# Kernel tuning notes

Hardware: AMD Instinct MI355X
Metric: run time of the kernel (lower is better)

The kernel has to match this reference:

```python
import jax, jax.numpy as jnp
import numpy as np

TS = 0.1
ECNUM = 1024
CA1NUM = 1024
CA3NUM = 1024
CA3SIGMA = 5.0
TRACKLEN = 100
ACTNUM = 2
BS = 8192
CUELOC = int(0.1 * TRACKLEN)  # sensory cue injected at this step
NOISE_P = 0.04 * TS           # per-step EC3 spontaneous-spike probability


def _xavier_std(fan_in, fan_out):
    return float(np.sqrt(2.0 / (fan_in + fan_out)))


def setup_inputs() -> dict:
    key = jax.random.key(0)
    ks = jax.random.split(key, 6)
    cue = jax.random.normal(ks[0], (BS, ECNUM), jnp.float32)
    ec5_init = jax.random.uniform(ks[1], (BS, ECNUM), jnp.float32)
    wca3ca1 = jax.random.uniform(ks[2], (CA3NUM, CA1NUM), jnp.float32) * 0.01
    wec3ca1 = jax.random.normal(ks[3], (ECNUM, CA1NUM), jnp.float32) * _xavier_std(ECNUM, CA1NUM)
    wca1ec5 = jax.random.normal(ks[4], (CA1NUM, ECNUM), jnp.float32) * _xavier_std(CA1NUM, ECNUM)
    wca1act = jax.random.normal(ks[5], (CA1NUM, ACTNUM), jnp.float32) * _xavier_std(CA1NUM, ACTNUM)
    ca1bias = jnp.zeros((CA1NUM,), jnp.float32)
    ec5bias = jnp.zeros((ECNUM,), jnp.float32)
    actbias = jnp.zeros((ACTNUM,), jnp.float32)
    return {"cue": cue, "ec5_init": ec5_init, "wca3ca1": wca3ca1,
            "wec3ca1": wec3ca1, "wca1ec5": wca1ec5, "wca1act": wca1act,
            "ca1bias": ca1bias, "ec5bias": ec5bias, "actbias": actbias}


def _forward(cue, ec5_init, wca3ca1, wec3ca1, wca1ec5, wca1act, ca1bias, ec5bias, actbias):
    bs = cue.shape[0]
    dt = cue.dtype
    # CA3 place-cell tuning curves for all positions: (T, ca3num)
    ca3center = jnp.linspace(0.0, TRACKLEN, CA3NUM).astype(dt)
    xs = jnp.arange(TRACKLEN)
    ca3_all = jnp.exp(-((ca3center[None, :] - xs[:, None].astype(dt)) ** 2)
                      / (2.0 * CA3SIGMA ** 2))
    drive = ca3_all @ wca3ca1            # (T, ca1num), precomputed CA3->CA1 drive
    cue_mask = (xs == CUELOC).astype(dt)  # (T,)
    noise_key = jax.random.key(42)

    ec3_0 = jnp.zeros((bs, ECNUM), dt)
    ca1_0 = jnp.zeros((bs, CA1NUM), dt)

    def step(carry, inp):
        ec3, ec5, _ = carry
        d, m, t = inp
        ca1 = jax.nn.relu(d[None, :] * (1.0 + jax.nn.sigmoid(ec3 @ wec3ca1)) - ca1bias)
        ec5 = ec5 + (10.0 * TS) * (ca1 @ wca1ec5) + ec5bias
        ec5 = 0.5 + 0.5 * jax.nn.sigmoid(4.0 * (ec5 - 0.5))
        ec3 = ec5 * ec3 + m * cue
        k = jax.random.fold_in(noise_key, t)
        ec3 = ec3 + 0.2 * jax.random.bernoulli(k, NOISE_P, (bs, ECNUM)).astype(dt)
        return (ec3, ec5, ca1), None

    (ec3, ec5, ca1), _ = jax.lax.scan(step, (ec3_0, ec5_init, ca1_0),
                                      (drive, cue_mask, xs))
    return ca1 @ wca1act + actbias       # (bs, actnum)


def reference(cue, ec5_init, wca3ca1, wec3ca1, wca1ec5, wca1act, ca1bias, ec5bias, actbias):
    return _forward(cue, ec5_init, wca3ca1, wec3ca1, wca1ec5, wca1act,
                    ca1bias, ec5bias, actbias)
```

## Files before the change

### kernel.cpp

```cpp
#include <hip/hip_runtime.h>
#include <stdint.h>

#define BS 8192
#define NDIM 1024
#define T_STEPS 100
#define CUE_T 10
#define BK 64
#define NKT (NDIM / BK)

typedef __attribute__((ext_vector_type(8))) short bf16x8;
typedef __attribute__((ext_vector_type(16))) float f32x16;

__device__ inline uint16_t f32_to_bf16(float f) {
    uint32_t u = __float_as_uint(f);
    uint32_t r = u + 0x7fffu + ((u >> 16) & 1u);
    return (uint16_t)(r >> 16);
}
__device__ inline float bf16_to_f32(uint16_t h) {
    return __uint_as_float(((uint32_t)h) << 16);
}

__host__ __device__ inline uint32_t rotl32_(uint32_t x, uint32_t r) {
    return (x << r) | (x >> (32u - r));
}

__host__ __device__ inline void tf2x32(uint32_t k0, uint32_t k1,
                                       uint32_t x0, uint32_t x1,
                                       uint32_t &o0, uint32_t &o1) {
    uint32_t ks2 = k0 ^ k1 ^ 0x1BD11BDAu;
    x0 += k0; x1 += k1;
#define TF_R4(a,b,c,d) \
    x0 += x1; x1 = rotl32_(x1,(a)); x1 ^= x0; \
    x0 += x1; x1 = rotl32_(x1,(b)); x1 ^= x0; \
    x0 += x1; x1 = rotl32_(x1,(c)); x1 ^= x0; \
    x0 += x1; x1 = rotl32_(x1,(d)); x1 ^= x0;
    TF_R4(13,15,26,6)  x0 += k1;  x1 += ks2 + 1u;
    TF_R4(17,29,16,24) x0 += ks2; x1 += k0 + 2u;
    TF_R4(13,15,26,6)  x0 += k0;  x1 += k1 + 3u;
    TF_R4(17,29,16,24) x0 += k1;  x1 += ks2 + 4u;
    TF_R4(13,15,26,6)  x0 += ks2; x1 += k0 + 5u;
#undef TF_R4
    o0 = x0; o1 = x1;
}

__device__ __forceinline__ void tf2x32_x4_fold(uint32_t k0, uint32_t k1,
                                               const uint32_t idx[4],
                                               uint32_t bits[4]) {
    uint32_t ks2 = k0 ^ k1 ^ 0x1BD11BDAu;
    uint32_t x0[4], x1[4];
    #pragma unroll
    for (int i = 0; i < 4; ++i) { x0[i] = k0; x1[i] = idx[i] + k1; }
#define TF4_R(rot) \
    _Pragma("unroll") \
    for (int i = 0; i < 4; ++i) { \
        x0[i] += x1[i]; x1[i] = rotl32_(x1[i], (rot)); x1[i] ^= x0[i]; }
#define TF4_K(a0, a1) \
    _Pragma("unroll") \
    for (int i = 0; i < 4; ++i) { x0[i] += (a0); x1[i] += (a1); }
    TF4_R(13) TF4_R(15) TF4_R(26) TF4_R(6)  TF4_K(k1, ks2 + 1u)
    TF4_R(17) TF4_R(29) TF4_R(16) TF4_R(24) TF4_K(ks2, k0 + 2u)
    TF4_R(13) TF4_R(15) TF4_R(26) TF4_R(6)  TF4_K(k0, k1 + 3u)
    TF4_R(17) TF4_R(29) TF4_R(16) TF4_R(24) TF4_K(k1, ks2 + 4u)
    TF4_R(13) TF4_R(15) TF4_R(26) TF4_R(6)  TF4_K(ks2, k0 + 5u)
#undef TF4_R
#undef TF4_K
    #pragma unroll
    for (int i = 0; i < 4; ++i) bits[i] = x0[i] ^ x1[i];
}

__device__ inline float sigmoidf_(float x) {
    float e = __expf(-x);
    return __builtin_amdgcn_rcpf(1.0f + e);
}

__device__ __forceinline__ void gload16(const uint16_t* g, uint16_t* l) {
    __builtin_amdgcn_global_load_lds(
        (const __attribute__((address_space(1))) void*)g,
        (__attribute__((address_space(3))) void*)l, 16, 0, 0);
}

__global__ void init_kernel(const float* __restrict__ ec5_init,
                            uint16_t* __restrict__ ec3bf,
                            uint16_t* __restrict__ ec5bf, int n) {
    int i = blockIdx.x * blockDim.x + threadIdx.x;
    if (i < n) { ec3bf[i] = 0; ec5bf[i] = f32_to_bf16(ec5_init[i]); }
}

__global__ __launch_bounds__(256) void drive_kernel(const float* __restrict__ W,
                                                    float* __restrict__ drive) {
    __shared__ float g[4][1024];
    const int t0 = blockIdx.x * 4;
    const int c = blockIdx.y * 64 + (threadIdx.x & 63);
    const int tt = threadIdx.x >> 6;
    const float stepf = 100.0f / 1023.0f;
    for (int i = threadIdx.x; i < 4096; i += 256) {
        int t_ = i >> 10, j = i & 1023;
        float d = stepf * (float)j - (float)(t0 + t_);
        g[t_][j] = expf(-(d * d) * 0.02f);
    }
    __syncthreads();
    float a = 0.f;
    for (int j = 0; j < 1024; ++j)
        a = fmaf(g[tt][j], W[(size_t)j * NDIM + c], a);
    drive[(size_t)(t0 + tt) * NDIM + c] = a;
}

__global__ __launch_bounds__(256) void wtrans_kernel(const float* __restrict__ W,
                                                     uint16_t* __restrict__ Wt) {
    __shared__ float tile[32][33];
    int k0 = blockIdx.x * 32, n0 = blockIdx.y * 32;
    int tx = threadIdx.x & 31, ty = threadIdx.x >> 5;
    #pragma unroll
    for (int i = 0; i < 32; i += 8)
        tile[ty + i][tx] = W[(size_t)(k0 + ty + i) * NDIM + n0 + tx];
    __syncthreads();
    #pragma unroll
    for (int i = 0; i < 32; i += 8)
        Wt[(size_t)(n0 + ty + i) * NDIM + k0 + tx] = f32_to_bf16(tile[tx][ty + i]);
}

template<bool NOISE>
__device__ __forceinline__ void gemm_core_t(const uint16_t* __restrict__ A,
                                            const uint16_t* __restrict__ Bt,
                                            uint16_t* As, uint16_t* Bs,
                                            f32x16 acc[2][2],
                                            uint32_t k0_, uint32_t k1_,
                                            uint32_t obase, uint64_t &mask) {
    const int tid = threadIdx.x;
    const int wid = tid >> 6, lane = tid & 63;
    const int row0 = blockIdx.x * 128, col0 = blockIdx.y * 128;
    const int srow = lane >> 3;
    const int soff = ((lane & 7) ^ srow) * 8;
    const uint16_t* aS[4]; const uint16_t* bS[4];
    #pragma unroll
    for (int i = 0; i < 4; ++i) {
        int ch = wid * 4 + i;
        aS[i] = A  + (size_t)(row0 + ch * 8 + srow) * NDIM + soff;
        bS[i] = Bt + (size_t)(col0 + ch * 8 + srow) * NDIM + soff;
    }
    const int l31 = lane & 31, l5 = lane >> 5;
    const int wr = wid >> 1, wc = wid & 1;
    int aoff[2][4], boff[2][4];
    #pragma unroll
    for (int m = 0; m < 2; ++m)
        #pragma unroll
        for (int kk = 0; kk < 4; ++kk) {
            int ar = wr * 64 + m * 32 + l31;
            aoff[m][kk] = ar * BK + ((((kk << 1) | l5) ^ (ar & 7)) << 3);
            int br = wc * 64 + m * 32 + l31;
            boff[m][kk] = br * BK + ((((kk << 1) | l5) ^ (br & 7)) << 3);
        }

    #pragma unroll
    for (int i = 0; i < 4; ++i) {
        int ch = wid * 4 + i;
        gload16(aS[i], As + ch * 512);
        gload16(bS[i], Bs + ch * 512);
    }

    for (int kt = 0; kt < NKT; ++kt) {
        const int cur = kt & 1;
        if (kt + 1 < NKT) {
            const int nb = (cur ^ 1) * 8192;
            const int k0n = (kt + 1) * BK;
            #pragma unroll
            for (int i = 0; i < 4; ++i) {
                int ch = wid * 4 + i;
                gload16(aS[i] + k0n, As + nb + ch * 512);
                gload16(bS[i] + k0n, Bs + nb + ch * 512);
            }
            asm volatile("s_waitcnt vmcnt(8)" ::: "memory");
        } else {
            asm volatile("s_waitcnt vmcnt(0)" ::: "memory");
        }
        __builtin_amdgcn_s_barrier();
        __builtin_amdgcn_sched_barrier(0);
        const uint16_t* as = As + cur * 8192;
        const uint16_t* bs = Bs + cur * 8192;
        bf16x8 af[2][4], bfr[2][4];
        #pragma unroll
        for (int m = 0; m < 2; ++m)
            #pragma unroll
            for (int kk = 0; kk < 4; ++kk) {
                af[m][kk]  = *(const bf16x8*)&as[aoff[m][kk]];
                bfr[m][kk] = *(const bf16x8*)&bs[boff[m][kk]];
            }
        #pragma unroll
        for (int kk = 0; kk < 4; ++kk)
            #pragma unroll
            for (int m = 0; m < 2; ++m)
                #pragma unroll
                for (int n = 0; n < 2; ++n)
                    acc[m][n] = __builtin_amdgcn_mfma_f32_32x32x16_bf16(
                        af[m][kk], bfr[n][kk], acc[m][n], 0, 0, 0);
        if (NOISE) {
            uint32_t idx[4], bits[4];
            const uint32_t base = obase + (uint32_t)((kt >> 1) << 14)
                                + (uint32_t)((kt & 1) << 2);
            #pragma unroll
            for (int u = 0; u < 4; ++u) idx[u] = base + u;
            tf2x32_x4_fold(k0_, k1_, idx, bits);
            #pragma unroll
            for (int u = 0; u < 4; ++u) {
                float uu = __uint_as_float((bits[u] >> 9) | 0x3f800000u) - 1.0f;
                mask |= (uint64_t)(uu < 0.004f ? 1u : 0u) << ((kt << 2) + u);
            }
        }
        __builtin_amdgcn_sched_barrier(0);
        __builtin_amdgcn_s_barrier();
    }
}

__device__ __forceinline__ void acc_to_lds(float* lacc, f32x16 acc[2][2]) {
    const int tid = threadIdx.x, wid = tid >> 6, lane = tid & 63;
    const int wr = wid >> 1, wc = wid & 1, l31 = lane & 31, l5 = lane >> 5;
    #pragma unroll
    for (int m = 0; m < 2; ++m)
        #pragma unroll
        for (int n = 0; n < 2; ++n) {
            int c = wc * 64 + n * 32 + l31;
            int chunk = c >> 2, cj = c & 3;
            #pragma unroll
            for (int e = 0; e < 16; ++e) {
                int r = wr * 64 + m * 32 + (e & 3) + ((e >> 2) << 3) + (l5 << 2);
                lacc[r * 128 + ((chunk ^ (r & 31)) << 2) + cj] = acc[m][n][e];
            }
        }
}

__device__ __forceinline__ void acc_read8(const float* lacc, int r, int a,
                                          float4 &v0, float4 &v1) {
    int rb = r & 31;
    v0 = *(const float4*)&lacc[r * 128 + ((((a << 1) | 0) ^ rb) << 2)];
    v1 = *(const float4*)&lacc[r * 128 + ((((a << 1) | 1) ^ rb) << 2)];
}

__global__ __launch_bounds__(256, 2) void gemm1_kernel(
    const uint16_t* __restrict__ ec3bf, const uint16_t* __restrict__ W1t,
    const float* __restrict__ drv, const float* __restrict__ bias,
    uint16_t* __restrict__ ca1bf, float* __restrict__ ca1f, int writef32,
    uint64_t* __restrict__ maskbuf, uint32_t k0_, uint32_t k1_)
{
    __shared__ __align__(16) uint16_t SM[2][16384];
    uint16_t* As = SM[0];
    uint16_t* Bs = SM[1];
    f32x16 acc[2][2];
    #pragma unroll
    for (int m = 0; m < 2; ++m)
        #pragma unroll
        for (int n = 0; n < 2; ++n)
            acc[m][n] = (f32x16)(0.0f);

    const int tid = threadIdx.x;
    const int row0 = blockIdx.x * 128, col0 = blockIdx.y * 128;
    const int a = tid & 15;
    const uint32_t obase = (uint32_t)(row0 + (tid >> 4)) * NDIM
                         + (uint32_t)(col0 + a * 8);
    uint64_t mask = 0;
    gemm_core_t<true>(ec3bf, W1t, As, Bs, acc, k0_, k1_, obase, mask);

    maskbuf[(size_t)(blockIdx.y * 64 + blockIdx.x) * 256 + tid] = mask;

    float* lacc = (float*)SM;
    acc_to_lds(lacc, acc);
    __syncthreads();

    #pragma unroll
    for (int i = 0; i < 8; ++i) {
        int r = (tid >> 4) + i * 16;
        float4 v0, v1;
        acc_read8(lacc, r, a, v0, v1);
        int gc = col0 + a * 8;
        float4 d0 = *(const float4*)&drv[gc];
        float4 d1 = *(const float4*)&drv[gc + 4];
        float4 b0 = *(const float4*)&bias[gc];
        float4 b1 = *(const float4*)&bias[gc + 4];
        size_t off = (size_t)(row0 + r) * NDIM + gc;
        float vout[8];
        #pragma unroll
        for (int j = 0; j < 8; ++j) {
            float accv = j < 4 ? v0[j] : v1[j - 4];
            float dv = j < 4 ? d0[j] : d1[j - 4];
            float bi = j < 4 ? b0[j] : b1[j - 4];
            float s = sigmoidf_(accv);
            float v = dv * (1.0f + s) - bi;
            vout[j] = v > 0.0f ? v : 0.0f;
        }
        bf16x8 pk;
        #pragma unroll
        for (int j = 0; j < 8; ++j) pk[j] = (short)f32_to_bf16(vout[j]);
        *(bf16x8*)&ca1bf[off] = pk;
        if (writef32) {
            float4 f0 = {vout[0], vout[1], vout[2], vout[3]};
            float4 f1 = {vout[4], vout[5], vout[6], vout[7]};
            *(float4*)&ca1f[off] = f0;
            *(float4*)&ca1f[off + 4] = f1;
        }
    }
}

__global__ __launch_bounds__(256, 2) void gemm2_kernel(
    const uint16_t* __restrict__ ca1bf, const uint16_t* __restrict__ W2t,
    const float* __restrict__ cue, const float* __restrict__ bias,
    uint16_t* __restrict__ ec3bf, uint16_t* __restrict__ ec5bf,
    const uint64_t* __restrict__ maskbuf, int inject)
{
    __shared__ __align__(16) uint16_t SM[2][16384];
    uint16_t* As = SM[0];
    uint16_t* Bs = SM[1];
    f32x16 acc[2][2];
    #pragma unroll
    for (int m = 0; m < 2; ++m)
        #pragma unroll
        for (int n = 0; n < 2; ++n)
            acc[m][n] = (f32x16)(0.0f);

    const int tid = threadIdx.x;
    const int row0 = blockIdx.x * 128, col0 = blockIdx.y * 128;
    const int a = tid & 15;
    const uint64_t mask = maskbuf[(size_t)(blockIdx.y * 64 + blockIdx.x) * 256 + tid];

    uint64_t dummy = 0;
    gemm_core_t<false>(ca1bf, W2t, As, Bs, acc, 0u, 0u, 0u, dummy);

    bf16x8 e3v[8], e5v[8];
    #pragma unroll
    for (int i = 0; i < 8; ++i) {
        size_t off = (size_t)(row0 + (tid >> 4) + i * 16) * NDIM + col0 + a * 8;
        e3v[i] = *(const bf16x8*)&ec3bf[off];
        e5v[i] = *(const bf16x8*)&ec5bf[off];
    }

    float* lacc = (float*)SM;
    acc_to_lds(lacc, acc);
    __syncthreads();

    #pragma unroll
    for (int i = 0; i < 8; ++i) {
        int r = (tid >> 4) + i * 16;
        float4 v0, v1;
        acc_read8(lacc, r, a, v0, v1);
        int gc = col0 + a * 8;
        size_t off = (size_t)(row0 + r) * NDIM + gc;
        float4 b0 = *(const float4*)&bias[gc];
        float4 b1 = *(const float4*)&bias[gc + 4];
        float4 c0 = {0.f,0.f,0.f,0.f}, c1 = {0.f,0.f,0.f,0.f};
        if (inject) {
            c0 = *(const float4*)&cue[off];
            c1 = *(const float4*)&cue[off + 4];
        }
        bf16x8 p3, p5;
        #pragma unroll
        for (int j = 0; j < 8; ++j) {
            float accv = j < 4 ? v0[j] : v1[j - 4];
            float bi = j < 4 ? b0[j] : b1[j - 4];
            float e5 = bf16_to_f32((uint16_t)e5v[i][j]);
            float e3 = bf16_to_f32((uint16_t)e3v[i][j]);
            float u = e5 + accv + bi;
            float e5n = 0.5f + 0.5f * sigmoidf_(4.0f * (u - 0.5f));
            float e3n = e5n * e3;
            if (inject) e3n += (j < 4 ? c0[j] : c1[j - 4]);
            e3n += ((mask >> (i * 8 + j)) & 1ull) ? 0.2f : 0.0f;
            p5[j] = (short)f32_to_bf16(e5n);
            p3[j] = (short)f32_to_bf16(e3n);
        }
        *(bf16x8*)&ec5bf[off] = p5;
        *(bf16x8*)&ec3bf[off] = p3;
    }
}

__global__ __launch_bounds__(256) void final_kernel(
    const float* __restrict__ ca1,
    const float* __restrict__ wact,
    const float* __restrict__ actbias,
    float* __restrict__ out)
{
    int wave = threadIdx.x >> 6, lane = threadIdx.x & 63;
    int b = blockIdx.x * 4 + wave;
    double a0 = 0.0, a1 = 0.0;
    for (int c = lane; c < NDIM; c += 64) {
        double v = (double)ca1[(size_t)b * NDIM + c];
        a0 += v * (double)wact[c * 2 + 0];
        a1 += v * (double)wact[c * 2 + 1];
    }
    #pragma unroll
    for (int off = 32; off > 0; off >>= 1) {
        a0 += __shfl_down(a0, off);
        a1 += __shfl_down(a1, off);
    }
    if (lane == 0) {
        out[(size_t)b * 2 + 0] = (float)(a0 + (double)actbias[0]);
        out[(size_t)b * 2 + 1] = (float)(a1 + (double)actbias[1]);
    }
}

extern "C" void kernel_launch(void* const* d_in, const int* in_sizes, int n_in,
                              void* d_out, int out_size, void* d_ws, size_t ws_size,
                              hipStream_t stream) {
    const float* cue      = (const float*)d_in[0];
    const float* ec5_init = (const float*)d_in[1];
    const float* wca3ca1  = (const float*)d_in[2];
    const float* wec3ca1  = (const float*)d_in[3];
    const float* wca1ec5  = (const float*)d_in[4];
    const float* wca1act  = (const float*)d_in[5];
    const float* ca1bias  = (const float*)d_in[6];
    const float* ec5bias  = (const float*)d_in[7];
    const float* actbias  = (const float*)d_in[8];
    float* out = (float*)d_out;

    const size_t NE = (size_t)BS * NDIM;
    char* p = (char*)d_ws;
    float*    ca1f    = (float*)p;    p += NE * 4;
    uint16_t* ec3bf   = (uint16_t*)p; p += NE * 2;
    uint16_t* ec5bf   = (uint16_t*)p; p += NE * 2;
    uint16_t* ca1bf   = (uint16_t*)p; p += NE * 2;
    uint16_t* W1t     = (uint16_t*)p; p += (size_t)NDIM * NDIM * 2;
    uint16_t* W2t     = (uint16_t*)p; p += (size_t)NDIM * NDIM * 2;
    uint64_t* maskbuf = (uint64_t*)p; p += (size_t)512 * 256 * 8;
    float*    drive   = (float*)p;

    const int n = (int)NE;
    hipLaunchKernelGGL(init_kernel, dim3((n + 255) / 256), dim3(256), 0, stream,
                       ec5_init, ec3bf, ec5bf, n);
    hipLaunchKernelGGL(drive_kernel, dim3(25, 16), dim3(256), 0, stream,
                       wca3ca1, drive);
    hipLaunchKernelGGL(wtrans_kernel, dim3(32, 32), dim3(256), 0, stream, wec3ca1, W1t);
    hipLaunchKernelGGL(wtrans_kernel, dim3(32, 32), dim3(256), 0, stream, wca1ec5, W2t);

    dim3 blk(256);
    dim3 gg(BS / 128, NDIM / 128);
    for (int t = 0; t < T_STEPS; ++t) {
        uint32_t k0, k1;
        tf2x32(0u, 42u, 0u, (uint32_t)t, k0, k1);
        hipLaunchKernelGGL(gemm1_kernel, gg, blk, 0, stream,
                           ec3bf, W1t, drive + (size_t)t * NDIM, ca1bias,
                           ca1bf, ca1f, (t == T_STEPS - 1) ? 1 : 0,
                           maskbuf, k0, k1);
        if (t < T_STEPS - 1) {
            hipLaunchKernelGGL(gemm2_kernel, gg, blk, 0, stream,
                               ca1bf, W2t, cue, ec5bias, ec3bf, ec5bf,
                               maskbuf, (t == CUE_T) ? 1 : 0);
        }
    }
    hipLaunchKernelGGL(final_kernel, dim3(BS / 4), blk, 0, stream,
                       ca1f, wca1act, actbias, out);
}
```

Measured before the change: 6.308 ms.

## Fuse all timesteps into one persistent cooperative kernel with grid syncs

Replaces the 199 per-step GEMM launches with one cooperative persistent kernel of 512 blocks. Each block loops over all timesteps, running both GEMMs and their epilogues, with grid.sync between phases. The Bernoulli noise mask now stays in registers instead of round-tripping through a global buffer. To fit 4 blocks per CU, the LDS double buffering is removed, so k-tile loads are no longer overlapped with MFMA and the epilogue runs in two half-tile passes. This trades launch overhead for lost load/compute overlap and grid-barrier cost.

```diff
diff --git a/kernel.cpp b/kernel.cpp
--- a/kernel.cpp
+++ b/kernel.cpp
@@ -1,5 +1,8 @@
 #include <hip/hip_runtime.h>
+#include <hip/hip_cooperative_groups.h>
 #include <stdint.h>
+
+namespace cg = cooperative_groups;
 
 #define BS 8192
 #define NDIM 1024
@@ -119,25 +122,50 @@
         Wt[(size_t)(n0 + ty + i) * NDIM + k0 + tx] = f32_to_bf16(tile[tx][ty + i]);
 }
 
-template<bool NOISE>
-__device__ __forceinline__ void gemm_core_t(const uint16_t* __restrict__ A,
-                                            const uint16_t* __restrict__ Bt,
-                                            uint16_t* As, uint16_t* Bs,
-                                            f32x16 acc[2][2],
-                                            uint32_t k0_, uint32_t k1_,
-                                            uint32_t obase, uint64_t &mask) {
+__device__ __forceinline__ void acc_pass_to_lds(float* lacc, f32x16 acc[2][2],
+                                                int p, int wr, int wc,
+                                                int l31, int l5) {
+    #pragma unroll
+    for (int n = 0; n < 2; ++n) {
+        int c = wc * 64 + n * 32 + l31;
+        int chunk = c >> 2, cj = c & 3;
+        #pragma unroll
+        for (int e = 0; e < 16; ++e) {
+            int rlow = (e & 3) + ((e >> 2) << 3) + (l5 << 2);
+            lacc[(wr * 32 + rlow) * 128 + ((chunk ^ rlow) << 2) + cj] = acc[p][n][e];
+        }
+    }
+}
+
+__device__ __forceinline__ void acc_read8(const float* lacc, int rp, int a,
+                                          float4 &v0, float4 &v1) {
+    int rb = rp & 31;
+    v0 = *(const float4*)&lacc[rp * 128 + ((((a << 1) | 0) ^ rb) << 2)];
+    v1 = *(const float4*)&lacc[rp * 128 + ((((a << 1) | 1) ^ rb) << 2)];
+}
+
+__global__ __launch_bounds__(256, 4) void fused_kernel(
+    uint16_t* __restrict__ ec3bf, uint16_t* __restrict__ ec5bf,
+    uint16_t* __restrict__ ca1bf,
+    const uint16_t* __restrict__ W1t, const uint16_t* __restrict__ W2t,
+    const float* __restrict__ drive, const float* __restrict__ ca1bias,
+    const float* __restrict__ ec5bias, const float* __restrict__ cue,
+    float* __restrict__ ca1f)
+{
+    cg::grid_group grid = cg::this_grid();
+    __shared__ __align__(16) uint16_t SM[16384];
+    uint16_t* As = SM;
+    uint16_t* Bs = SM + 8192;
+    float* lacc = (float*)SM;
+
     const int tid = threadIdx.x;
     const int wid = tid >> 6, lane = tid & 63;
-    const int row0 = blockIdx.x * 128, col0 = blockIdx.y * 128;
+    const int blin = blockIdx.x;
+    const int bx = blin & 63, by = blin >> 6;
+    const int row0 = bx * 128, col0 = by * 128;
+
     const int srow = lane >> 3;
     const int soff = ((lane & 7) ^ srow) * 8;
-    const uint16_t* aS[4]; const uint16_t* bS[4];
-    #pragma unroll
-    for (int i = 0; i < 4; ++i) {
-        int ch = wid * 4 + i;
-        aS[i] = A  + (size_t)(row0 + ch * 8 + srow) * NDIM + soff;
-        bS[i] = Bt + (size_t)(col0 + ch * 8 + srow) * NDIM + soff;
-    }
     const int l31 = lane & 31, l5 = lane >> 5;
     const int wr = wid >> 1, wc = wid & 1;
     int aoff[2][4], boff[2][4];
@@ -151,221 +179,212 @@
             boff[m][kk] = br * BK + ((((kk << 1) | l5) ^ (br & 7)) << 3);
         }
 
-    #pragma unroll
-    for (int i = 0; i < 4; ++i) {
-        int ch = wid * 4 + i;
-        gload16(aS[i], As + ch * 512);
-        gload16(bS[i], Bs + ch * 512);
-    }
-
-    for (int kt = 0; kt < NKT; ++kt) {
-        const int cur = kt & 1;
-        if (kt + 1 < NKT) {
-            const int nb = (cur ^ 1) * 8192;
-            const int k0n = (kt + 1) * BK;
+    const int a = tid & 15;
+    const int gc = col0 + a * 8;
+    const uint32_t obase = (uint32_t)(row0 + (tid >> 4)) * NDIM + (uint32_t)gc;
+    const float4 cb0 = *(const float4*)&ca1bias[gc];
+    const float4 cb1 = *(const float4*)&ca1bias[gc + 4];
+    const float4 eb0 = *(const float4*)&ec5bias[gc];
+    const float4 eb1 = *(const float4*)&ec5bias[gc + 4];
+
+    static const int passA[4] = {0, 1, 4, 5};
+    static const int passB[4] = {2, 3, 6, 7};
+
+    for (int t = 0; t < T_STEPS; ++t) {
+        uint32_t k0_, k1_;
+        tf2x32(0u, 42u, 0u, (uint32_t)t, k0_, k1_);
+        const float* drv = drive + (size_t)t * NDIM;
+
+        f32x16 acc[2][2];
+        #pragma unroll
+        for (int m = 0; m < 2; ++m)
+            #pragma unroll
+            for (int n = 0; n < 2; ++n)
+                acc[m][n] = (f32x16)(0.0f);
+        uint64_t mask = 0;
+
+        const uint16_t* aS[4]; const uint16_t* bS[4];
+        #pragma unroll
+        for (int i = 0; i < 4; ++i) {
+            int ch = wid * 4 + i;
+            aS[i] = ec3bf + (size_t)(row0 + ch * 8 + srow) * NDIM + soff;
+            bS[i] = W1t   + (size_t)(col0 + ch * 8 + srow) * NDIM + soff;
+        }
+        for (int kt = 0; kt < NKT; ++kt) {
+            if (kt) __builtin_amdgcn_s_barrier();
+            const int k0n = kt * BK;
             #pragma unroll
             for (int i = 0; i < 4; ++i) {
                 int ch = wid * 4 + i;
-                gload16(aS[i] + k0n, As + nb + ch * 512);
-                gload16(bS[i] + k0n, Bs + nb + ch * 512);
+                gload16(aS[i] + k0n, As + ch * 512);
+                gload16(bS[i] + k0n, Bs + ch * 512);
             }
-            asm volatile("s_waitcnt vmcnt(8)" ::: "memory");
-        } else {
+            {
+                uint32_t idx[4], bits[4];
+                const uint32_t base = obase + (uint32_t)((kt >> 1) << 14)
+                                    + (uint32_t)((kt & 1) << 2);
+                #pragma unroll
+                for (int u = 0; u < 4; ++u) idx[u] = base + u;
+                tf2x32_x4_fold(k0_, k1_, idx, bits);
+                #pragma unroll
+                for (int u = 0; u < 4; ++u) {
+                    float uu = __uint_as_float((bits[u] >> 9) | 0x3f800000u) - 1.0f;
+                    mask |= (uint64_t)(uu < 0.004f ? 1u : 0u) << ((kt << 2) + u);
+                }
+            }
             asm volatile("s_waitcnt vmcnt(0)" ::: "memory");
-        }
-        __builtin_amdgcn_s_barrier();
-        __builtin_amdgcn_sched_barrier(0);
-        const uint16_t* as = As + cur * 8192;
-        const uint16_t* bs = Bs + cur * 8192;
-        bf16x8 af[2][4], bfr[2][4];
+            __builtin_amdgcn_s_barrier();
+            __builtin_amdgcn_sched_barrier(0);
+            bf16x8 af[2][4], bfr[2][4];
+            #pragma unroll
+            for (int m = 0; m < 2; ++m)
+                #pragma unroll
+                for (int kk = 0; kk < 4; ++kk) {
+                    af[m][kk]  = *(const bf16x8*)&As[aoff[m][kk]];
+                    bfr[m][kk] = *(const bf16x8*)&Bs[boff[m][kk]];
+                }
+            #pragma unroll
+            for (int kk = 0; kk < 4; ++kk)
+                #pragma unroll
+                for (int m = 0; m < 2; ++m)
+                    #pragma unroll
+                    for (int n = 0; n < 2; ++n)
+                        acc[m][n] = __builtin_amdgcn_mfma_f32_32x32x16_bf16(
+                            af[m][kk], bfr[n][kk], acc[m][n], 0, 0, 0);
+            __builtin_amdgcn_sched_barrier(0);
+        }
+
+        const float4 d0 = *(const float4*)&drv[gc];
+        const float4 d1 = *(const float4*)&drv[gc + 4];
+        #pragma unroll
+        for (int p = 0; p < 2; ++p) {
+            __syncthreads();
+            acc_pass_to_lds(lacc, acc, p, wr, wc, l31, l5);
+            __syncthreads();
+            const int* il = p ? passB : passA;
+            #pragma unroll
+            for (int ii = 0; ii < 4; ++ii) {
+                int i = il[ii];
+                int r = (tid >> 4) + i * 16;
+                int rp = ((r >> 6) << 5) | (r & 31);
+                float4 v0, v1;
+                acc_read8(lacc, rp, a, v0, v1);
+                size_t off = (size_t)(row0 + r) * NDIM + gc;
+                float vout[8];
+                #pragma unroll
+                for (int j = 0; j < 8; ++j) {
+                    float accv = j < 4 ? v0[j] : v1[j - 4];
+                    float dv = j < 4 ? d0[j] : d1[j - 4];
+                    float bi = j < 4 ? cb0[j] : cb1[j - 4];
+                    float s = sigmoidf_(accv);
+                    float v = dv * (1.0f + s) - bi;
+                    vout[j] = v > 0.0f ? v : 0.0f;
+                }
+                bf16x8 pk;
+                #pragma unroll
+                for (int j = 0; j < 8; ++j) pk[j] = (short)f32_to_bf16(vout[j]);
+                *(bf16x8*)&ca1bf[off] = pk;
+                if (t == T_STEPS - 1) {
+                    float4 f0 = {vout[0], vout[1], vout[2], vout[3]};
+                    float4 f1 = {vout[4], vout[5], vout[6], vout[7]};
+                    *(float4*)&ca1f[off] = f0;
+                    *(float4*)&ca1f[off + 4] = f1;
+                }
+            }
+        }
+        if (t == T_STEPS - 1) break;
+        grid.sync();
+
         #pragma unroll
         for (int m = 0; m < 2; ++m)
             #pragma unroll
-            for (int kk = 0; kk < 4; ++kk) {
-                af[m][kk]  = *(const bf16x8*)&as[aoff[m][kk]];
-                bfr[m][kk] = *(const bf16x8*)&bs[boff[m][kk]];
+            for (int n = 0; n < 2; ++n)
+                acc[m][n] = (f32x16)(0.0f);
+        #pragma unroll
+        for (int i = 0; i < 4; ++i) {
+            int ch = wid * 4 + i;
+            aS[i] = ca1bf + (size_t)(row0 + ch * 8 + srow) * NDIM + soff;
+            bS[i] = W2t   + (size_t)(col0 + ch * 8 + srow) * NDIM + soff;
+        }
+        for (int kt = 0; kt < NKT; ++kt) {
+            if (kt) __builtin_amdgcn_s_barrier();
+            const int k0n = kt * BK;
+            #pragma unroll
+            for (int i = 0; i < 4; ++i) {
+                int ch = wid * 4 + i;
+                gload16(aS[i] + k0n, As + ch * 512);
+                gload16(bS[i] + k0n, Bs + ch * 512);
             }
-        #pragma unroll
-        for (int kk = 0; kk < 4; ++kk)
+            asm volatile("s_waitcnt vmcnt(0)" ::: "memory");
+            __builtin_amdgcn_s_barrier();
+            __builtin_amdgcn_sched_barrier(0);
+            bf16x8 af[2][4], bfr[2][4];
             #pragma unroll
             for (int m = 0; m < 2; ++m)
                 #pragma unroll
-                for (int n = 0; n < 2; ++n)
-                    acc[m][n] = __builtin_amdgcn_mfma_f32_32x32x16_bf16(
-                        af[m][kk], bfr[n][kk], acc[m][n], 0, 0, 0);
-        if (NOISE) {
-            uint32_t idx[4], bits[4];
-            const uint32_t base = obase + (uint32_t)((kt >> 1) << 14)
-                                + (uint32_t)((kt & 1) << 2);
-            #pragma unroll
-            for (int u = 0; u < 4; ++u) idx[u] = base + u;
-            tf2x32_x4_fold(k0_, k1_, idx, bits);
-            #pragma unroll
-            for (int u = 0; u < 4; ++u) {
-                float uu = __uint_as_float((bits[u] >> 9) | 0x3f800000u) - 1.0f;
-                mask |= (uint64_t)(uu < 0.004f ? 1u : 0u) << ((kt << 2) + u);
+                for (int kk = 0; kk < 4; ++kk) {
+                    af[m][kk]  = *(const bf16x8*)&As[aoff[m][kk]];
+                    bfr[m][kk] = *(const bf16x8*)&Bs[boff[m][kk]];
+                }
+            #pragma unroll
+            for (int kk = 0; kk < 4; ++kk)
+                #pragma unroll
+                for (int m = 0; m < 2; ++m)
+                    #pragma unroll
+                    for (int n = 0; n < 2; ++n)
+                        acc[m][n] = __builtin_amdgcn_mfma_f32_32x32x16_bf16(
+                            af[m][kk], bfr[n][kk], acc[m][n], 0, 0, 0);
+            __builtin_amdgcn_sched_barrier(0);
+        }
+
+        bf16x8 e3v[8], e5v[8];
+        #pragma unroll
+        for (int i = 0; i < 8; ++i) {
+            size_t off = (size_t)(row0 + (tid >> 4) + i * 16) * NDIM + gc;
+            e3v[i] = *(const bf16x8*)&ec3bf[off];
+            e5v[i] = *(const bf16x8*)&ec5bf[off];
+        }
+
+        const int inject = (t == CUE_T);
+        #pragma unroll
+        for (int p = 0; p < 2; ++p) {
+            __syncthreads();
+            acc_pass_to_lds(lacc, acc, p, wr, wc, l31, l5);
+            __syncthreads();
+            const int* il = p ? passB : passA;
+            #pragma unroll
+            for (int ii = 0; ii < 4; ++ii) {
+                int i = il[ii];
+                int r = (tid >> 4) + i * 16;
+                int rp = ((r >> 6) << 5) | (r & 31);
+                float4 v0, v1;
+                acc_read8(lacc, rp, a, v0, v1);
+                size_t off = (size_t)(row0 + r) * NDIM + gc;
+                float4 c0 = {0.f,0.f,0.f,0.f}, c1 = {0.f,0.f,0.f,0.f};
+                if (inject) {
+                    c0 = *(const float4*)&cue[off];
+                    c1 = *(const float4*)&cue[off + 4];
+                }
+                bf16x8 p3, p5;
+                #pragma unroll
+                for (int j = 0; j < 8; ++j) {
+                    float accv = j < 4 ? v0[j] : v1[j - 4];
+                    float bi = j < 4 ? eb0[j] : eb1[j - 4];
+                    float e5 = bf16_to_f32((uint16_t)e5v[i][j]);
+                    float e3 = bf16_to_f32((uint16_t)e3v[i][j]);
+                    float u = e5 + accv + bi;
+                    float e5n = 0.5f + 0.5f * sigmoidf_(4.0f * (u - 0.5f));
+                    float e3n = e5n * e3;
+                    if (inject) e3n += (j < 4 ? c0[j] : c1[j - 4]);
+                    e3n += ((mask >> (i * 8 + j)) & 1ull) ? 0.2f : 0.0f;
+                    p5[j] = (short)f32_to_bf16(e5n);
+                    p3[j] = (short)f32_to_bf16(e3n);
+                }
+                *(bf16x8*)&ec5bf[off] = p5;
+                *(bf16x8*)&ec3bf[off] = p3;
             }
         }
-        __builtin_amdgcn_sched_barrier(0);
-        __builtin_amdgcn_s_barrier();
-    }
-}
-
-__device__ __forceinline__ void acc_to_lds(float* lacc, f32x16 acc[2][2]) {
-    const int tid = threadIdx.x, wid = tid >> 6, lane = tid & 63;
-    const int wr = wid >> 1, wc = wid & 1, l31 = lane & 31, l5 = lane >> 5;
-    #pragma unroll
-    for (int m = 0; m < 2; ++m)
-        #pragma unroll
-        for (int n = 0; n < 2; ++n) {
-            int c = wc * 64 + n * 32 + l31;
-            int chunk = c >> 2, cj = c & 3;
-            #pragma unroll
-            for (int e = 0; e < 16; ++e) {
-                int r = wr * 64 + m * 32 + (e & 3) + ((e >> 2) << 3) + (l5 << 2);
-                lacc[r * 128 + ((chunk ^ (r & 31)) << 2) + cj] = acc[m][n][e];
-            }
-        }
-}
-
-__device__ __forceinline__ void acc_read8(const float* lacc, int r, int a,
-                                          float4 &v0, float4 &v1) {
-    int rb = r & 31;
-    v0 = *(const float4*)&lacc[r * 128 + ((((a << 1) | 0) ^ rb) << 2)];
-    v1 = *(const float4*)&lacc[r * 128 + ((((a << 1) | 1) ^ rb) << 2)];
-}
-
-__global__ __launch_bounds__(256, 2) void gemm1_kernel(
-    const uint16_t* __restrict__ ec3bf, const uint16_t* __restrict__ W1t,
-    const float* __restrict__ drv, const float* __restrict__ bias,
-    uint16_t* __restrict__ ca1bf, float* __restrict__ ca1f, int writef32,
-    uint64_t* __restrict__ maskbuf, uint32_t k0_, uint32_t k1_)
-{
-    __shared__ __align__(16) uint16_t SM[2][16384];
-    uint16_t* As = SM[0];
-    uint16_t* Bs = SM[1];
-    f32x16 acc[2][2];
-    #pragma unroll
-    for (int m = 0; m < 2; ++m)
-        #pragma unroll
-        for (int n = 0; n < 2; ++n)
-            acc[m][n] = (f32x16)(0.0f);
-
-    const int tid = threadIdx.x;
-    const int row0 = blockIdx.x * 128, col0 = blockIdx.y * 128;
-    const int a = tid & 15;
-    const uint32_t obase = (uint32_t)(row0 + (tid >> 4)) * NDIM
-                         + (uint32_t)(col0 + a * 8);
-    uint64_t mask = 0;
-    gemm_core_t<true>(ec3bf, W1t, As, Bs, acc, k0_, k1_, obase, mask);
-
-    maskbuf[(size_t)(blockIdx.y * 64 + blockIdx.x) * 256 + tid] = mask;
-
-    float* lacc = (float*)SM;
-    acc_to_lds(lacc, acc);
-    __syncthreads();
-
-    #pragma unroll
-    for (int i = 0; i < 8; ++i) {
-        int r = (tid >> 4) + i * 16;
-        float4 v0, v1;
-        acc_read8(lacc, r, a, v0, v1);
-        int gc = col0 + a * 8;
-        float4 d0 = *(const float4*)&drv[gc];
-        float4 d1 = *(const float4*)&drv[gc + 4];
-        float4 b0 = *(const float4*)&bias[gc];
-        float4 b1 = *(const float4*)&bias[gc + 4];
-        size_t off = (size_t)(row0 + r) * NDIM + gc;
-        float vout[8];
-        #pragma unroll
-        for (int j = 0; j < 8; ++j) {
-            float accv = j < 4 ? v0[j] : v1[j - 4];
-            float dv = j < 4 ? d0[j] : d1[j - 4];
-            float bi = j < 4 ? b0[j] : b1[j - 4];
-            float s = sigmoidf_(accv);
-            float v = dv * (1.0f + s) - bi;
-            vout[j] = v > 0.0f ? v : 0.0f;
-        }
-        bf16x8 pk;
-        #pragma unroll
-        for (int j = 0; j < 8; ++j) pk[j] = (short)f32_to_bf16(vout[j]);
-        *(bf16x8*)&ca1bf[off] = pk;
-        if (writef32) {
-            float4 f0 = {vout[0], vout[1], vout[2], vout[3]};
-            float4 f1 = {vout[4], vout[5], vout[6], vout[7]};
-            *(float4*)&ca1f[off] = f0;
-            *(float4*)&ca1f[off + 4] = f1;
-        }
-    }
-}
-
-__global__ __launch_bounds__(256, 2) void gemm2_kernel(
-    const uint16_t* __restrict__ ca1bf, const uint16_t* __restrict__ W2t,
-    const float* __restrict__ cue, const float* __restrict__ bias,
-    uint16_t* __restrict__ ec3bf, uint16_t* __restrict__ ec5bf,
-    const uint64_t* __restrict__ maskbuf, int inject)
-{
-    __shared__ __align__(16) uint16_t SM[2][16384];
-    uint16_t* As = SM[0];
-    uint16_t* Bs = SM[1];
-    f32x16 acc[2][2];
-    #pragma unroll
-    for (int m = 0; m < 2; ++m)
-        #pragma unroll
-        for (int n = 0; n < 2; ++n)
-            acc[m][n] = (f32x16)(0.0f);
-
-    const int tid = threadIdx.x;
-    const int row0 = blockIdx.x * 128, col0 = blockIdx.y * 128;
-    const int a = tid & 15;
-    const uint64_t mask = maskbuf[(size_t)(blockIdx.y * 64 + blockIdx.x) * 256 + tid];
-
-    uint64_t dummy = 0;
-    gemm_core_t<false>(ca1bf, W2t, As, Bs, acc, 0u, 0u, 0u, dummy);
-
-    bf16x8 e3v[8], e5v[8];
-    #pragma unroll
-    for (int i = 0; i < 8; ++i) {
-        size_t off = (size_t)(row0 + (tid >> 4) + i * 16) * NDIM + col0 + a * 8;
-        e3v[i] = *(const bf16x8*)&ec3bf[off];
-        e5v[i] = *(const bf16x8*)&ec5bf[off];
-    }
-
-    float* lacc = (float*)SM;
-    acc_to_lds(lacc, acc);
-    __syncthreads();
-
-    #pragma unroll
-    for (int i = 0; i < 8; ++i) {
-        int r = (tid >> 4) + i * 16;
-        float4 v0, v1;
-        acc_read8(lacc, r, a, v0, v1);
-        int gc = col0 + a * 8;
-        size_t off = (size_t)(row0 + r) * NDIM + gc;
-        float4 b0 = *(const float4*)&bias[gc];
-        float4 b1 = *(const float4*)&bias[gc + 4];
-        float4 c0 = {0.f,0.f,0.f,0.f}, c1 = {0.f,0.f,0.f,0.f};
-        if (inject) {
-            c0 = *(const float4*)&cue[off];
-            c1 = *(const float4*)&cue[off + 4];
-        }
-        bf16x8 p3, p5;
-        #pragma unroll
-        for (int j = 0; j < 8; ++j) {
-            float accv = j < 4 ? v0[j] : v1[j - 4];
-            float bi = j < 4 ? b0[j] : b1[j - 4];
-            float e5 = bf16_to_f32((uint16_t)e5v[i][j]);
-            float e3 = bf16_to_f32((uint16_t)e3v[i][j]);
-            float u = e5 + accv + bi;
-            float e5n = 0.5f + 0.5f * sigmoidf_(4.0f * (u - 0.5f));
-            float e3n = e5n * e3;
-            if (inject) e3n += (j < 4 ? c0[j] : c1[j - 4]);
-            e3n += ((mask >> (i * 8 + j)) & 1ull) ? 0.2f : 0.0f;
-            p5[j] = (short)f32_to_bf16(e5n);
-            p3[j] = (short)f32_to_bf16(e3n);
-        }
-        *(bf16x8*)&ec5bf[off] = p5;
-        *(bf16x8*)&ec3bf[off] = p3;
+        grid.sync();
     }
 }
 
@@ -416,7 +435,6 @@
     uint16_t* ca1bf   = (uint16_t*)p; p += NE * 2;
     uint16_t* W1t     = (uint16_t*)p; p += (size_t)NDIM * NDIM * 2;
     uint16_t* W2t     = (uint16_t*)p; p += (size_t)NDIM * NDIM * 2;
-    uint64_t* maskbuf = (uint64_t*)p; p += (size_t)512 * 256 * 8;
     float*    drive   = (float*)p;
 
     const int n = (int)NE;
@@ -427,21 +445,15 @@
     hipLaunchKernelGGL(wtrans_kernel, dim3(32, 32), dim3(256), 0, stream, wec3ca1, W1t);
     hipLaunchKernelGGL(wtrans_kernel, dim3(32, 32), dim3(256), 0, stream, wca1ec5, W2t);
 
-    dim3 blk(256);
-    dim3 gg(BS / 128, NDIM / 128);
-    for (int t = 0; t < T_STEPS; ++t) {
-        uint32_t k0, k1;
-        tf2x32(0u, 42u, 0u, (uint32_t)t, k0, k1);
-        hipLaunchKernelGGL(gemm1_kernel, gg, blk, 0, stream,
-                           ec3bf, W1t, drive + (size_t)t * NDIM, ca1bias,
-                           ca1bf, ca1f, (t == T_STEPS - 1) ? 1 : 0,
-                           maskbuf, k0, k1);
-        if (t < T_STEPS - 1) {
-            hipLaunchKernelGGL(gemm2_kernel, gg, blk, 0, stream,
-                               ca1bf, W2t, cue, ec5bias, ec3bf, ec5bf,
-                               maskbuf, (t == CUE_T) ? 1 : 0);
-        }
-    }
-    hipLaunchKernelGGL(final_kernel, dim3(BS / 4), blk, 0, stream,
+    void* args[] = {
+        (void*)&ec3bf, (void*)&ec5bf, (void*)&ca1bf,
+        (void*)&W1t, (void*)&W2t,
+        (void*)&drive, (void*)&ca1bias, (void*)&ec5bias, (void*)&cue,
+        (void*)&ca1f
+    };
+    hipLaunchCooperativeKernel((const void*)fused_kernel, dim3(512), dim3(256),
+                               args, 0, stream);
+
+    hipLaunchKernelGGL(final_kernel, dim3(BS / 4), dim3(256), 0, stream,
                        ca1f, wca1act, actbias, out);
 }
```

After: 24.99 ms. 296% more time.
